# Optimization experiments

Measured on AMD Instinct MI355X. Metric: run time of the kernel, lower is better.

## Reference

```python
import jax, jax.numpy as jnp
import numpy as np

D_MODEL = 2048; D_STATE = 128; D_CONV = 4; EXPAND = 2
HEADDIM = 64; NGROUPS = 1; CHUNK = 256
D_INNER = EXPAND * D_MODEL          # 4096
NHEADS = D_INNER // HEADDIM         # 64
HG = NHEADS // NGROUPS              # heads per group
CONV_DIM = D_INNER + 2 * NGROUPS * D_STATE          # 4352
D_IN_PROJ = 2 * D_INNER + 2 * NGROUPS * D_STATE + NHEADS  # 8512
BATCH = 2; SEQLEN = 2048
EPS = 1e-5


def setup_inputs() -> dict:
    ks = jax.random.split(jax.random.key(0), 8)
    u = jax.random.normal(ks[0], (BATCH, SEQLEN, D_MODEL), jnp.float32)
    in_proj_w = jax.random.normal(ks[1], (D_IN_PROJ, D_MODEL), jnp.float32) * D_MODEL ** -0.5
    conv_w = jax.random.normal(ks[2], (CONV_DIM, D_CONV), jnp.float32) * D_CONV ** -0.5
    conv_b = jax.random.normal(ks[3], (CONV_DIM,), jnp.float32) * 0.1
    # dt_bias init exactly as in the module: inv softplus of dt ~ U(log(1e-3), log(1e-1))
    dt = jnp.exp(jax.random.uniform(ks[4], (NHEADS,), jnp.float32)
                 * (np.float32(np.log(0.1)) - np.float32(np.log(0.001))) + np.float32(np.log(0.001)))
    dt = jnp.clip(dt, 1e-4, None)
    dt_bias = dt + jnp.log(-jnp.expm1(-dt))
    A_log = jnp.log(jax.random.uniform(ks[5], (NHEADS,), jnp.float32, minval=1.0, maxval=16.0))
    D_skip = jnp.ones((NHEADS,), jnp.float32)
    norm_w = jnp.ones((D_INNER,), jnp.float32)
    out_proj_w = jax.random.normal(ks[6], (D_MODEL, D_INNER), jnp.float32) * D_INNER ** -0.5
    return dict(u=u, in_proj_w=in_proj_w, conv_w=conv_w, conv_b=conv_b,
                dt_bias=dt_bias, A_log=A_log, D_skip=D_skip,
                norm_w=norm_w, out_proj_w=out_proj_w)


def _mamba2(u, in_proj_w, conv_w, conv_b, dt_bias, A_log, D_skip, norm_w, out_proj_w):
    b, l, _ = u.shape
    nc = l // CHUNK
    zxbcdt = u @ in_proj_w.T                                   # (b,l,d_in_proj)
    z = zxbcdt[..., :D_INNER]                                  # gate
    xBC = zxbcdt[..., D_INNER:D_INNER + CONV_DIM]
    dt = jax.nn.softplus(zxbcdt[..., D_INNER + CONV_DIM:] + dt_bias)  # (b,l,h)
    # causal depthwise conv1d (padding d_conv-1, truncated to seqlen) + SiLU
    xp = jnp.pad(xBC, ((0, 0), (D_CONV - 1, 0), (0, 0)))
    conv = conv_b + sum(conv_w[:, k] * xp[:, k:k + l, :] for k in range(D_CONV))
    xBC = jax.nn.silu(conv)
    x = xBC[..., :D_INNER].reshape(b, l, NHEADS, HEADDIM)
    Bm = xBC[..., D_INNER:D_INNER + NGROUPS * D_STATE].reshape(b, l, NGROUPS, D_STATE)
    Cm = xBC[..., D_INNER + NGROUPS * D_STATE:].reshape(b, l, NGROUPS, D_STATE)
    A = -jnp.exp(A_log)                                        # (h,)
    # ---- SSD chunked scan ----
    xc = x.reshape(b, nc, CHUNK, NGROUPS, HG, HEADDIM)         # (b,c,s,g,H,p)
    dtc = dt.reshape(b, nc, CHUNK, NGROUPS, HG)                # (b,c,s,g,H)
    Bc = Bm.reshape(b, nc, CHUNK, NGROUPS, D_STATE)            # (b,c,s,g,n)
    Cc = Cm.reshape(b, nc, CHUNK, NGROUPS, D_STATE)
    dA = jnp.transpose(dtc * A.reshape(NGROUPS, HG), (0, 3, 4, 1, 2))  # (b,g,H,c,s)
    dA_cs = jnp.cumsum(dA, axis=-1)                            # (b,g,H,c,s)
    # intra-chunk: L[i,j] = exp(sum_{j<k<=i} dA_k), lower-triangular (diag=1)
    seg = dA_cs[..., :, None] - dA_cs[..., None, :]            # (b,g,H,c,l,s)
    tri = jnp.tril(jnp.ones((CHUNK, CHUNK), bool))
    Lmat = jnp.where(tri, jnp.exp(seg), 0.0)
    xdt = xc * dtc[..., None]                                  # (b,c,s,g,H,p)
    CB = jnp.einsum('bclgn,bcsgn->bcgls', Cc, Bc)
    Y_diag = jnp.einsum('bcgls,bgHcls,bcsgHp->bclgHp', CB, Lmat, xdt)
    # chunk states and inter-chunk recurrence
    decay_states = jnp.exp(dA_cs[..., -1:] - dA_cs)            # (b,g,H,c,s)
    states = jnp.einsum('bcsgn,bgHcs,bcsgHp->bcgHpn', Bc, decay_states, xdt)
    chunk_decay = jnp.exp(dA_cs[..., -1])                      # (b,g,H,c)

    def step(carry, inp):
        st, dec = inp
        return carry * dec[..., None, None] + st, carry

    _, prev = jax.lax.scan(step, jnp.zeros_like(states[:, 0]),
                           (jnp.moveaxis(states, 1, 0), jnp.moveaxis(chunk_decay, -1, 0)))
    prev = jnp.moveaxis(prev, 0, 1)                            # (b,c,g,H,p,n) state entering chunk
    Y_off = jnp.einsum('bclgn,bcgHpn,bgHcl->bclgHp', Cc, prev, jnp.exp(dA_cs))
    y = (Y_diag + Y_off).reshape(b, l, NHEADS, HEADDIM) + x * D_skip[None, None, :, None]
    y = y.reshape(b, l, D_INNER)
    # gated RMSNorm: gate first (norm_before_gate=False), groupwise rms (ngroups=1 -> full)
    y = y * jax.nn.silu(z)
    yg = y.reshape(b, l, NGROUPS, D_INNER // NGROUPS)
    yg = yg * jax.lax.rsqrt(jnp.mean(yg * yg, axis=-1, keepdims=True) + EPS)
    y = yg.reshape(b, l, D_INNER) * norm_w
    return y @ out_proj_w.T                                    # (b,l,d_model)


def reference(u, in_proj_w, conv_w, conv_b, dt_bias, A_log, D_skip, norm_w, out_proj_w):
    return _mamba2(u, in_proj_w, conv_w, conv_b, dt_bias, A_log, D_skip, norm_w, out_proj_w)
```

## Files before the change

kernel.cpp:

```cpp
#include <hip/hip_runtime.h>
#include <hip/hip_bf16.h>


#define D_MODEL   2048
#define D_STATE   128
#define HEADDIM   64
#define CHUNK     256
#define D_INNER   4096
#define NHEADS    64
#define CONV_DIM  4352
#define D_IN_PROJ 8512
#define SEQLEN    2048
#define NC        8
#define ROWSTOT   4096
#define NPAD      8576
#define RMS_EPS   1e-5f

#define OFF_WIN   0ull
#define OFF_XBF   0ull
#define OFF_PREV  0ull
#define OFF_WOUT  16777216ull
#define OFF_UBF   35127296ull
#define OFF_DTV   35127296ull
#define OFF_DACS  36175872ull
#define OFF_BBF   37224448ull
#define OFF_CBF   38273024ull
#define OFF_CB    39321600ull
#define OFF_BT    43515904ull
#define OFF_XBC   51904512ull
#define OFF_STATE 51904512ull
#define OFF_ZBF   87556096ull
#define OFF_DTRAW 121110528ull
#define OFF_YBUF  121110528ull
#define WS_NEEDED 154664960ull

#define N4_U    2097152l
#define N4_WIN  4390912l

typedef __hip_bfloat16 bf16;
typedef __bf16 bfrag8 __attribute__((ext_vector_type(8)));
typedef float  f32x4v __attribute__((ext_vector_type(4)));

__device__ __forceinline__ f32x4v mfma16(bfrag8 a, bfrag8 b, f32x4v c) {
  return __builtin_amdgcn_mfma_f32_16x16x32_bf16(a, b, c, 0, 0, 0);
}

__device__ __forceinline__ void gload_lds16(const void* g, void* l) {
  __builtin_amdgcn_global_load_lds((const __attribute__((address_space(1))) void*)g,
                                   (__attribute__((address_space(3))) void*)l, 16, 0, 0);
}

__device__ __forceinline__ bf16 f2b(float x) { return __float2bfloat16(x); }
__device__ __forceinline__ float b2f(bf16 x) { return __bfloat162float(x); }
__device__ __forceinline__ float siluf(float x) { return x / (1.f + __expf(-x)); }

__global__ __launch_bounds__(256) void cast_all_kernel(const float* __restrict__ u,
    const float* __restrict__ w_in,
    bf16* __restrict__ u_bf, bf16* __restrict__ win_bf) {
  long i = (long)blockIdx.x * 256 + threadIdx.x;
  if (i < N4_U) {
    float4 v = ((const float4*)u)[i];
    bf16* o = u_bf + i * 4;
    o[0] = f2b(v.x); o[1] = f2b(v.y); o[2] = f2b(v.z); o[3] = f2b(v.w);
  } else if (i < N4_U + N4_WIN) {
    long e = (i - N4_U) * 4;
    long row = e / D_MODEL;
    bf16* o = win_bf + e;
    if (row < D_IN_PROJ) {
      float4 v = *(const float4*)(w_in + e);
      o[0] = f2b(v.x); o[1] = f2b(v.y); o[2] = f2b(v.z); o[3] = f2b(v.w);
    } else {
      bf16 z = f2b(0.f);
      o[0] = z; o[1] = z; o[2] = z; o[3] = z;
    }
  }
}

__global__ __launch_bounds__(256) void cast_kernel(const float* __restrict__ in,
                                                   bf16* __restrict__ out, long n4) {
  long i = (long)blockIdx.x * 256 + threadIdx.x;
  if (i >= n4) return;
  float4 v = ((const float4*)in)[i];
  bf16* o = out + i * 4;
  o[0] = f2b(v.x); o[1] = f2b(v.y); o[2] = f2b(v.z); o[3] = f2b(v.w);
}

__global__ __launch_bounds__(512) void gemm1_kernel(const bf16* __restrict__ A,
                                                    const bf16* __restrict__ B,
                                                    bf16* __restrict__ zb,
                                                    bf16* __restrict__ xbc,
                                                    float* __restrict__ dtraw) {
  int pid = blockIdx.x;
  int t = pid & 63, s = pid >> 6;
  int sm = s / 9, sn = s % 9;
  int xcd = t & 7, j8 = t >> 3;
  int tm = sm * 8 + (xcd >> 1) * 2 + (j8 & 1);
  int tn = sn * 8 + (xcd & 1) * 4 + (j8 >> 1);
  if (tn >= 67) return;
  long row0 = (long)tm * 256, col0 = (long)tn * 128;

  __shared__ __align__(16) bf16 As[2 * 256 * 32];
  __shared__ __align__(16) bf16 Bs[2 * 128 * 32];
  int tid = threadIdx.x, lane = tid & 63, w = tid >> 6;
  int wr = w >> 1, wc = w & 1, r16 = lane & 15, q = lane >> 4;
  const int K = D_MODEL;
  f32x4v zero4 = {0.f, 0.f, 0.f, 0.f};
  f32x4v acc[4][4];
#pragma unroll
  for (int i = 0; i < 4; ++i)
#pragma unroll
    for (int j = 0; j < 4; ++j) acc[i][j] = zero4;

  for (int kt = 0; kt < K; kt += 64) {
    __syncthreads();
#pragma unroll
    for (int j = 0; j < 4; ++j) {
      int ci = j * 512 + tid;
      int half = ci >> 10, cj = ci & 1023;
      int r = cj >> 2, ko = half * 32 + (cj & 3) * 8;
      gload_lds16(A + (row0 + r) * (long)K + kt + ko,
                  (char*)As + j * 8192 + w * 1024);
    }
#pragma unroll
    for (int j = 0; j < 2; ++j) {
      int ci = j * 512 + tid;
      int half = ci >> 9, cj = ci & 511;
      int r = cj >> 2, ko = half * 32 + (cj & 3) * 8;
      gload_lds16(B + (col0 + r) * (long)K + kt + ko,
                  (char*)Bs + j * 8192 + w * 1024);
    }
    __syncthreads();
#pragma unroll
    for (int ks = 0; ks < 2; ++ks) {
      const bf16* Ab = As + ks * 8192;
      const bf16* Bb = Bs + ks * 4096;
      bfrag8 af[4], bfv[4];
#pragma unroll
      for (int i = 0; i < 4; ++i) af[i]  = *(const bfrag8*)(Ab + (wr * 64 + i * 16 + r16) * 32 + q * 8);
#pragma unroll
      for (int i = 0; i < 4; ++i) bfv[i] = *(const bfrag8*)(Bb + (wc * 64 + i * 16 + r16) * 32 + q * 8);
#pragma unroll
      for (int i = 0; i < 4; ++i)
#pragma unroll
        for (int j = 0; j < 4; ++j) acc[i][j] = mfma16(af[i], bfv[j], acc[i][j]);
    }
  }
#pragma unroll
  for (int i = 0; i < 4; ++i)
#pragma unroll
    for (int j = 0; j < 4; ++j) {
      long col = col0 + wc * 64 + j * 16 + r16;
#pragma unroll
      for (int r = 0; r < 4; ++r) {
        long row = row0 + wr * 64 + i * 16 + q * 4 + r;
        float v = acc[i][j][r];
        if (col < D_INNER)                       zb[row * D_INNER + col] = f2b(v);
        else if (col < D_INNER + CONV_DIM)       xbc[row * CONV_DIM + (col - D_INNER)] = f2b(v);
        else if (col < D_IN_PROJ)                dtraw[row * NHEADS + (col - D_INNER - CONV_DIM)] = v;
      }
    }
}

__global__ __launch_bounds__(256) void gemm2_kernel(const bf16* __restrict__ A,
                                                    const bf16* __restrict__ B,
                                                    float* __restrict__ C) {
  int pid = blockIdx.x;
  int t = pid & 63, s = pid >> 6;
  int sm = s >> 1, sn = s & 1;
  int xcd = t & 7, j8 = t >> 3;
  int tm = sm * 8 + (xcd >> 1) * 2 + (j8 & 1);
  int tn = sn * 8 + (xcd & 1) * 4 + (j8 >> 1);
  long row0 = (long)tm * 128, col0 = (long)tn * 128;

  __shared__ __align__(16) bf16 As[2 * 128 * 32];
  __shared__ __align__(16) bf16 Bs[2 * 128 * 32];
  int tid = threadIdx.x, lane = tid & 63, w = tid >> 6;
  int wr = w >> 1, wc = w & 1, r16 = lane & 15, q = lane >> 4;
  const int K = D_INNER, ldc = D_MODEL;
  f32x4v zero4 = {0.f, 0.f, 0.f, 0.f};
  f32x4v acc[4][4];
#pragma unroll
  for (int i = 0; i < 4; ++i)
#pragma unroll
    for (int j = 0; j < 4; ++j) acc[i][j] = zero4;

  for (int kt = 0; kt < K; kt += 64) {
    __syncthreads();
#pragma unroll
    for (int j = 0; j < 4; ++j) {
      int ci = (j * 4 + w) * 64 + lane;
      int half = ci >> 9, cj = ci & 511;
      int r = cj >> 2, ko = half * 32 + (cj & 3) * 8;
      gload_lds16(A + (row0 + r) * (long)K + kt + ko,
                  (char*)As + (j * 4 + w) * 1024);
    }
#pragma unroll
    for (int j = 0; j < 4; ++j) {
      int ci = (j * 4 + w) * 64 + lane;
      int half = ci >> 9, cj = ci & 511;
      int r = cj >> 2, ko = half * 32 + (cj & 3) * 8;
      gload_lds16(B + (col0 + r) * (long)K + kt + ko,
                  (char*)Bs + (j * 4 + w) * 1024);
    }
    __syncthreads();
#pragma unroll
    for (int ks = 0; ks < 2; ++ks) {
      const bf16* Ab = As + ks * 4096;
      const bf16* Bb = Bs + ks * 4096;
      bfrag8 af[4], bfv[4];
#pragma unroll
      for (int i = 0; i < 4; ++i) af[i]  = *(const bfrag8*)(Ab + (wr * 64 + i * 16 + r16) * 32 + q * 8);
#pragma unroll
      for (int i = 0; i < 4; ++i) bfv[i] = *(const bfrag8*)(Bb + (wc * 64 + i * 16 + r16) * 32 + q * 8);
#pragma unroll
      for (int i = 0; i < 4; ++i)
#pragma unroll
        for (int j = 0; j < 4; ++j) acc[i][j] = mfma16(af[i], bfv[j], acc[i][j]);
    }
  }
#pragma unroll
  for (int i = 0; i < 4; ++i)
#pragma unroll
    for (int j = 0; j < 4; ++j)
#pragma unroll
      for (int r = 0; r < 4; ++r) {
        long row = row0 + wr * 64 + i * 16 + q * 4 + r;
        long col = col0 + wc * 64 + j * 16 + r16;
        C[row * ldc + col] = acc[i][j][r];
      }
}

__global__ __launch_bounds__(256) void dt_scan_kernel(const float* __restrict__ dtraw,
    const float* __restrict__ dt_bias, const float* __restrict__ A_log,
    float* __restrict__ dtv_buf, float* __restrict__ dacs_buf) {
  int blk = blockIdx.x;
  int c = blk & 7, h = (blk >> 3) & 63, b = blk >> 9;
  int s = threadIdx.x, lane = s & 63, w = s >> 6;
  long row = (long)b * SEQLEN + c * CHUNK + s;
  float raw = dtraw[row * NHEADS + h] + dt_bias[h];
  float dtv = fmaxf(raw, 0.f) + log1pf(__expf(-fabsf(raw)));
  float A = -__expf(A_log[h]);
  float x = dtv * A;
#pragma unroll
  for (int off = 1; off < 64; off <<= 1) {
    float y = __shfl_up(x, off);
    if (lane >= off) x += y;
  }
  __shared__ __align__(16) float wsum[4];
  if (lane == 63) wsum[w] = x;
  __syncthreads();
  float pre = 0.f;
#pragma unroll
  for (int i = 0; i < 4; ++i) pre += (i < w) ? wsum[i] : 0.f;
  long o = ((long)(b * NHEADS + h) * NC + c) * CHUNK + s;
  dtv_buf[o] = dtv;
  dacs_buf[o] = x + pre;
}

__global__ __launch_bounds__(256) void conv_kernel(const bf16* __restrict__ xbc,
    const float* __restrict__ conv_w, const float* __restrict__ conv_b,
    bf16* __restrict__ xo, bf16* __restrict__ Bo, bf16* __restrict__ Co,
    bf16* __restrict__ BT) {
  int cidx = blockIdx.x * 256 + threadIdx.x;
  int l0 = blockIdx.y * 8, b = blockIdx.z;
  float4 wv = *(const float4*)(conv_w + cidx * 4);
  float bias = conv_b[cidx];
  const bf16* base = xbc + (long)b * SEQLEN * CONV_DIM + cidx;
  float win[11];
#pragma unroll
  for (int k = 0; k < 11; ++k) {
    int ls = l0 - 3 + k;
    win[k] = (ls >= 0) ? b2f(base[(long)ls * CONV_DIM]) : 0.f;
  }
  int cgrp = (cidx < D_INNER) ? 0 : ((cidx < D_INNER + D_STATE) ? 1 : 2);
  int n = cidx - D_INNER;
  int n2 = cidx - D_INNER - D_STATE;
  int cch = l0 >> 8;
#pragma unroll
  for (int j = 0; j < 8; ++j) {
    float acc = bias + wv.x * win[j] + wv.y * win[j + 1] + wv.z * win[j + 2] + wv.w * win[j + 3];
    bf16 o = f2b(siluf(acc));
    int l = l0 + j;
    long rowo = (long)b * SEQLEN + l;
    if (cgrp == 0) {
      xo[rowo * D_INNER + cidx] = o;
    } else if (cgrp == 1) {
      Bo[rowo * D_STATE + n] = o;
      BT[(((long)b * NC + cch) * D_STATE + n) * CHUNK + (l & 255)] = o;
    } else {
      Co[rowo * D_STATE + n2] = o;
    }
  }
}

__global__ __launch_bounds__(256) void cb_kernel(const bf16* __restrict__ Cg,
                                                 const bf16* __restrict__ Bg,
                                                 float* __restrict__ CB) {
  int blk = blockIdx.x;
  int stile = blk & 3, bc = blk >> 2;
  int c = bc & 7, b = bc >> 3;
  int tid = threadIdx.x, lane = tid & 63, w = tid >> 6, r16 = lane & 15, q = lane >> 4;
  const bf16* Cb = Cg + ((long)b * SEQLEN + c * CHUNK) * D_STATE;
  const bf16* Bb = Bg + ((long)b * SEQLEN + c * CHUNK) * D_STATE;
  bfrag8 af[4][4];
#pragma unroll
  for (int lt = 0; lt < 4; ++lt)
#pragma unroll
    for (int kk = 0; kk < 4; ++kk)
      af[lt][kk] = *(const bfrag8*)(Cb + (long)(w * 64 + lt * 16 + r16) * D_STATE + kk * 32 + q * 8);
  float* CBb = CB + (long)bc * CHUNK * CHUNK;
  f32x4v zero4 = {0.f, 0.f, 0.f, 0.f};
  for (int st = stile * 4; st < stile * 4 + 4; ++st) {
    f32x4v acc[4] = {zero4, zero4, zero4, zero4};
#pragma unroll
    for (int kk = 0; kk < 4; ++kk) {
      bfrag8 bfv = *(const bfrag8*)(Bb + (long)(st * 16 + r16) * D_STATE + kk * 32 + q * 8);
#pragma unroll
      for (int lt = 0; lt < 4; ++lt) acc[lt] = mfma16(af[lt][kk], bfv, acc[lt]);
    }
#pragma unroll
    for (int lt = 0; lt < 4; ++lt)
#pragma unroll
      for (int r = 0; r < 4; ++r)
        CBb[(long)(w * 64 + lt * 16 + q * 4 + r) * CHUNK + st * 16 + r16] = acc[lt][r];
  }
}

__global__ __launch_bounds__(256) void ssm_diag_kernel(
    const bf16* __restrict__ xg, const bf16* __restrict__ BT,
    const float* __restrict__ CB, const float* __restrict__ dtv_buf,
    const float* __restrict__ dacs_buf, const float* __restrict__ Dskip,
    bf16* __restrict__ ybuf, float* __restrict__ states) {
  int blk = blockIdx.x;
  int h = blk & 63, cc = (blk >> 6) & 7, b = blk >> 9;
  int tid = threadIdx.x, lane = tid & 63, w = tid >> 6, r16 = lane & 15, q = lane >> 4;

  __shared__ __align__(16) __bf16 xT[HEADDIM][264];
  __shared__ __align__(16) float cs_s[CHUNK];
  __shared__ __align__(16) float dt_s[CHUNK];
  __shared__ __align__(16) float w_s[CHUNK];

  long hco = ((long)(b * NHEADS + h) * NC + cc) * CHUNK;
  cs_s[tid] = dacs_buf[hco + tid];
  dt_s[tid] = dtv_buf[hco + tid];
  __syncthreads();
  float cl_last = cs_s[CHUNK - 1];
  w_s[tid] = __expf(cl_last - cs_s[tid]) * dt_s[tid];

  const __bf16* xbase = (const __bf16*)(xg + ((long)b * SEQLEN + cc * CHUNK) * D_INNER + h * HEADDIM);
#pragma unroll
  for (int it = 0; it < 8; ++it) {
    int e = it * 256 + tid;
    int s = e >> 3, p0 = (e & 7) * 8;
    bfrag8 xv = *(const bfrag8*)(xbase + (long)s * D_INNER + p0);
#pragma unroll
    for (int j = 0; j < 8; ++j) xT[p0 + j][s] = xv[j];
  }
  __syncthreads();

  const float* CBchunk = CB + (long)(b * NC + cc) * CHUNK * CHUNK;
  const __bf16* BTc = (const __bf16*)(BT + (((long)b * NC + cc) * D_STATE) * CHUNK);
  f32x4v zero4 = {0.f, 0.f, 0.f, 0.f};
  f32x4v accY[4][4], accS[2][4];
#pragma unroll
  for (int i = 0; i < 4; ++i)
#pragma unroll
    for (int j = 0; j < 4; ++j) accY[i][j] = zero4;
#pragma unroll
  for (int i = 0; i < 2; ++i)
#pragma unroll
    for (int j = 0; j < 4; ++j) accS[i][j] = zero4;

  int l_row[4];
  const float* CBrow[4];
#pragma unroll
  for (int lt = 0; lt < 4; ++lt) {
    l_row[lt] = w * 64 + lt * 16 + r16;
    CBrow[lt] = CBchunk + (long)l_row[lt] * CHUNK;
  }

#pragma unroll 2
  for (int ks = 0; ks < 8; ++ks) {
    int s0 = ks * 32 + q * 8;
    float4 cs0 = *(const float4*)(cs_s + s0);
    float4 cs1 = *(const float4*)(cs_s + s0 + 4);
    float4 dt0 = *(const float4*)(dt_s + s0);
    float4 dt1 = *(const float4*)(dt_s + s0 + 4);
    float4 w0  = *(const float4*)(w_s + s0);
    float4 w1  = *(const float4*)(w_s + s0 + 4);
    float csv[8] = {cs0.x, cs0.y, cs0.z, cs0.w, cs1.x, cs1.y, cs1.z, cs1.w};
    float dtv8[8] = {dt0.x, dt0.y, dt0.z, dt0.w, dt1.x, dt1.y, dt1.z, dt1.w};
    float wv8[8]  = {w0.x, w0.y, w0.z, w0.w, w1.x, w1.y, w1.z, w1.w};

    bfrag8 xf[4];
#pragma unroll
    for (int pt = 0; pt < 4; ++pt) xf[pt] = *(const bfrag8*)(&xT[pt * 16 + r16][s0]);

#pragma unroll
    for (int lt = 0; lt < 4; ++lt) {
      int l = l_row[lt];
      float cs_l = cs_s[l];
      float4 cb0 = *(const float4*)(CBrow[lt] + s0);
      float4 cb1 = *(const float4*)(CBrow[lt] + s0 + 4);
      float cbv[8] = {cb0.x, cb0.y, cb0.z, cb0.w, cb1.x, cb1.y, cb1.z, cb1.w};
      bfrag8 pf;
#pragma unroll
      for (int j = 0; j < 8; ++j) {
        float v = (s0 + j <= l)
                    ? cbv[j] * __expf(fminf(cs_l - csv[j], 0.f)) * dtv8[j]
                    : 0.f;
        pf[j] = (__bf16)v;
      }
#pragma unroll
      for (int pt = 0; pt < 4; ++pt) accY[lt][pt] = mfma16(pf, xf[pt], accY[lt][pt]);
    }

#pragma unroll
    for (int nt = 0; nt < 2; ++nt) {
      int n = w * 32 + nt * 16 + r16;
      bfrag8 braw = *(const bfrag8*)(BTc + (long)n * CHUNK + s0);
      bfrag8 bwf;
#pragma unroll
      for (int j = 0; j < 8; ++j) bwf[j] = (__bf16)((float)braw[j] * wv8[j]);
#pragma unroll
      for (int pt = 0; pt < 4; ++pt) accS[nt][pt] = mfma16(bwf, xf[pt], accS[nt][pt]);
    }
  }

  float dsk = Dskip[h];
  bf16* ybase = ybuf + ((long)b * SEQLEN + cc * CHUNK) * D_INNER + h * HEADDIM;
#pragma unroll
  for (int lt = 0; lt < 4; ++lt)
#pragma unroll
    for (int pt = 0; pt < 4; ++pt)
#pragma unroll
      for (int r = 0; r < 4; ++r) {
        int lrow = w * 64 + lt * 16 + q * 4 + r;
        int pcol = pt * 16 + r16;
        ybase[(long)lrow * D_INNER + pcol] = f2b(accY[lt][pt][r] + (float)xT[pcol][lrow] * dsk);
      }
  float* sbase = states + (long)blk * (HEADDIM * D_STATE);
#pragma unroll
  for (int nt = 0; nt < 2; ++nt)
#pragma unroll
    for (int pt = 0; pt < 4; ++pt)
#pragma unroll
      for (int r = 0; r < 4; ++r)
        sbase[(long)(pt * 16 + r16) * D_STATE + w * 32 + nt * 16 + q * 4 + r] = accS[nt][pt][r];
}

__global__ __launch_bounds__(256) void state_scan_kernel(const float* __restrict__ states,
    const float* __restrict__ dacs, bf16* __restrict__ prevb) {
  int gid = blockIdx.x;
  int et = gid & 31, bh = gid >> 5;
  int h = bh & 63, b = bh >> 6;
  int e = et * 256 + threadIdx.x;
  float dec[NC];
#pragma unroll
  for (int c = 0; c < NC; ++c)
    dec[c] = __expf(dacs[((long)(b * NHEADS + h) * NC + c) * CHUNK + (CHUNK - 1)]);
  float carry = 0.f;
#pragma unroll
  for (int c = 0; c < NC; ++c) {
    long off = ((long)((b * NC + c) * NHEADS + h)) * (HEADDIM * D_STATE) + e;
    prevb[off] = f2b(carry);
    carry = carry * dec[c] + states[off];
  }
}

__global__ __launch_bounds__(256) void yoff_kernel(const bf16* __restrict__ Cg,
    const bf16* __restrict__ prevb, const float* __restrict__ dacs,
    bf16* __restrict__ ybuf) {
  int blk = blockIdx.x;
  int h = blk & 63, cc = (blk >> 6) & 7, b = blk >> 9;
  int tid = threadIdx.x, lane = tid & 63, w = tid >> 6, r16 = lane & 15, q = lane >> 4;
  __shared__ __align__(16) float cs_s[CHUNK];
  cs_s[tid] = dacs[((long)(b * NHEADS + h) * NC + cc) * CHUNK + tid];
  __syncthreads();
  const bf16* Cb = Cg + ((long)b * SEQLEN + cc * CHUNK) * D_STATE;
  const bf16* Pb = prevb + (long)blk * (HEADDIM * D_STATE);
  f32x4v zero4 = {0.f, 0.f, 0.f, 0.f};
  f32x4v acc[4][4];
#pragma unroll
  for (int i = 0; i < 4; ++i)
#pragma unroll
    for (int j = 0; j < 4; ++j) acc[i][j] = zero4;
#pragma unroll
  for (int kk = 0; kk < 4; ++kk) {
    bfrag8 bv[4];
#pragma unroll
    for (int pt = 0; pt < 4; ++pt)
      bv[pt] = *(const bfrag8*)(Pb + (long)(pt * 16 + r16) * D_STATE + kk * 32 + q * 8);
#pragma unroll
    for (int lt = 0; lt < 4; ++lt) {
      bfrag8 av = *(const bfrag8*)(Cb + (long)(w * 64 + lt * 16 + r16) * D_STATE + kk * 32 + q * 8);
#pragma unroll
      for (int pt = 0; pt < 4; ++pt) acc[lt][pt] = mfma16(av, bv[pt], acc[lt][pt]);
    }
  }
  bf16* ybase = ybuf + ((long)b * SEQLEN + cc * CHUNK) * D_INNER + h * HEADDIM;
#pragma unroll
  for (int lt = 0; lt < 4; ++lt)
#pragma unroll
    for (int pt = 0; pt < 4; ++pt)
#pragma unroll
      for (int r = 0; r < 4; ++r) {
        int lrow = w * 64 + lt * 16 + q * 4 + r;
        float ef = __expf(cs_s[lrow]);
        bf16* p = ybase + (long)lrow * D_INNER + pt * 16 + r16;
        *p = f2b(b2f(*p) + acc[lt][pt][r] * ef);
      }
}

__global__ __launch_bounds__(256) void gate_norm_kernel(bf16* __restrict__ ybuf,
    const bf16* __restrict__ zb, const float* __restrict__ norm_w) {
  int row = blockIdx.x, tid = threadIdx.x;
  bf16* y = ybuf + (long)row * D_INNER;
  const bf16* z = zb + (long)row * D_INNER;
  float v[16];
  float ss = 0.f;
#pragma unroll
  for (int i = 0; i < 2; ++i) {
    int e = tid * 16 + i * 8;
    bfrag8 yv = *(const bfrag8*)(y + e);
    bfrag8 zv = *(const bfrag8*)(z + e);
#pragma unroll
    for (int j = 0; j < 8; ++j) {
      float a = (float)yv[j] * siluf((float)zv[j]);
      v[i * 8 + j] = a;
      ss += a * a;
    }
  }
#pragma unroll
  for (int off = 32; off > 0; off >>= 1) ss += __shfl_down(ss, off);
  __shared__ __align__(16) float red[4];
  int lane = tid & 63, w = tid >> 6;
  if (lane == 0) red[w] = ss;
  __syncthreads();
  float tot = red[0] + red[1] + red[2] + red[3];
  float scale = rsqrtf(tot * (1.f / D_INNER) + RMS_EPS);
#pragma unroll
  for (int i = 0; i < 2; ++i) {
    int e = tid * 16 + i * 8;
    float4 w0 = *(const float4*)(norm_w + e);
    float4 w1 = *(const float4*)(norm_w + e + 4);
    bfrag8 o;
    o[0] = (__bf16)(v[i * 8 + 0] * scale * w0.x);
    o[1] = (__bf16)(v[i * 8 + 1] * scale * w0.y);
    o[2] = (__bf16)(v[i * 8 + 2] * scale * w0.z);
    o[3] = (__bf16)(v[i * 8 + 3] * scale * w0.w);
    o[4] = (__bf16)(v[i * 8 + 4] * scale * w1.x);
    o[5] = (__bf16)(v[i * 8 + 5] * scale * w1.y);
    o[6] = (__bf16)(v[i * 8 + 6] * scale * w1.z);
    o[7] = (__bf16)(v[i * 8 + 7] * scale * w1.w);
    *(bfrag8*)(y + e) = o;
  }
}

extern "C" void kernel_launch(void* const* d_in, const int* in_sizes, int n_in,
                              void* d_out, int out_size, void* d_ws, size_t ws_size,
                              hipStream_t stream) {
  if (ws_size < WS_NEEDED) return;

  const float* u       = (const float*)d_in[0];
  const float* w_in    = (const float*)d_in[1];
  const float* conv_w  = (const float*)d_in[2];
  const float* conv_b  = (const float*)d_in[3];
  const float* dt_bias = (const float*)d_in[4];
  const float* A_log   = (const float*)d_in[5];
  const float* Dskip   = (const float*)d_in[6];
  const float* norm_w  = (const float*)d_in[7];
  const float* w_out   = (const float*)d_in[8];
  float* out = (float*)d_out;

  char* ws = (char*)d_ws;
  bf16*  win_bf  = (bf16*)(ws + OFF_WIN);
  bf16*  x_bf    = (bf16*)(ws + OFF_XBF);
  bf16*  prevb   = (bf16*)(ws + OFF_PREV);
  bf16*  wout_bf = (bf16*)(ws + OFF_WOUT);
  bf16*  u_bf    = (bf16*)(ws + OFF_UBF);
  float* dtv     = (float*)(ws + OFF_DTV);
  float* dacs    = (float*)(ws + OFF_DACS);
  bf16*  B_bf    = (bf16*)(ws + OFF_BBF);
  bf16*  C_bf    = (bf16*)(ws + OFF_CBF);
  float* CBb     = (float*)(ws + OFF_CB);
  bf16*  BT_bf   = (bf16*)(ws + OFF_BT);
  bf16*  xbc_bf  = (bf16*)(ws + OFF_XBC);
  float* states  = (float*)(ws + OFF_STATE);
  bf16*  z_bf    = (bf16*)(ws + OFF_ZBF);
  float* dt_raw  = (float*)(ws + OFF_DTRAW);
  bf16*  ybuf    = (bf16*)(ws + OFF_YBUF);

  cast_all_kernel<<<25344, 256, 0, stream>>>(u, w_in, u_bf, win_bf);
  gemm1_kernel<<<1152, 512, 0, stream>>>(u_bf, win_bf, z_bf, xbc_bf, dt_raw);
  dt_scan_kernel<<<1024, 256, 0, stream>>>(dt_raw, dt_bias, A_log, dtv, dacs);
  conv_kernel<<<dim3(17, SEQLEN / 8, 2), 256, 0, stream>>>(xbc_bf, conv_w, conv_b, x_bf, B_bf, C_bf, BT_bf);
  cb_kernel<<<64, 256, 0, stream>>>(C_bf, B_bf, CBb);
  ssm_diag_kernel<<<1024, 256, 0, stream>>>(x_bf, BT_bf, CBb, dtv, dacs, Dskip, ybuf, states);
  state_scan_kernel<<<4096, 256, 0, stream>>>(states, dacs, prevb);
  yoff_kernel<<<1024, 256, 0, stream>>>(C_bf, prevb, dacs, ybuf);
  cast_kernel<<<8192, 256, 0, stream>>>(w_out, wout_bf, (long)D_MODEL * D_INNER / 4);
  gate_norm_kernel<<<ROWSTOT, 256, 0, stream>>>(ybuf, z_bf, norm_w);
  gemm2_kernel<<<512, 256, 0, stream>>>(ybuf, wout_bf, out);
}
```

Measured before the change: 590.5 us.

## Swizzle LDS tiles in both GEMMs and enlarge gemm2 tile to 256x128

Applies an XOR swizzle to the K-chunk offset when staging A and B tiles into shared memory, and applies the matching swizzle when reading fragments. This is meant to cut LDS bank conflicts on the 16-byte fragment reads in both GEMMs. gemm2 is also moved from 128x128 tiles with 256 threads to 256x128 tiles with 512 threads and half as many blocks. The larger tile increases reuse of the B tile, at the cost of fewer workgroups for occupancy and load balance.

```diff
diff --git a/kernel.cpp b/kernel.cpp
--- a/kernel.cpp
+++ b/kernel.cpp
@@ -85,6 +85,7 @@
   o[0] = f2b(v.x); o[1] = f2b(v.y); o[2] = f2b(v.z); o[3] = f2b(v.w);
 }
 
+
 __global__ __launch_bounds__(512) void gemm1_kernel(const bf16* __restrict__ A,
                                                     const bf16* __restrict__ B,
                                                     bf16* __restrict__ zb,
@@ -103,6 +104,7 @@
   __shared__ __align__(16) bf16 Bs[2 * 128 * 32];
   int tid = threadIdx.x, lane = tid & 63, w = tid >> 6;
   int wr = w >> 1, wc = w & 1, r16 = lane & 15, q = lane >> 4;
+  int qs = (q ^ ((r16 >> 1) & 3)) * 8;
   const int K = D_MODEL;
   f32x4v zero4 = {0.f, 0.f, 0.f, 0.f};
   f32x4v acc[4][4];
@@ -117,7 +119,8 @@
     for (int j = 0; j < 4; ++j) {
       int ci = j * 512 + tid;
       int half = ci >> 10, cj = ci & 1023;
-      int r = cj >> 2, ko = half * 32 + (cj & 3) * 8;
+      int r = cj >> 2;
+      int ko = half * 32 + ((cj & 3) ^ ((cj >> 3) & 3)) * 8;
       gload_lds16(A + (row0 + r) * (long)K + kt + ko,
                   (char*)As + j * 8192 + w * 1024);
     }
@@ -125,7 +128,8 @@
     for (int j = 0; j < 2; ++j) {
       int ci = j * 512 + tid;
       int half = ci >> 9, cj = ci & 511;
-      int r = cj >> 2, ko = half * 32 + (cj & 3) * 8;
+      int r = cj >> 2;
+      int ko = half * 32 + ((cj & 3) ^ ((cj >> 3) & 3)) * 8;
       gload_lds16(B + (col0 + r) * (long)K + kt + ko,
                   (char*)Bs + j * 8192 + w * 1024);
     }
@@ -136,9 +140,9 @@
       const bf16* Bb = Bs + ks * 4096;
       bfrag8 af[4], bfv[4];
 #pragma unroll
-      for (int i = 0; i < 4; ++i) af[i]  = *(const bfrag8*)(Ab + (wr * 64 + i * 16 + r16) * 32 + q * 8);
-#pragma unroll
-      for (int i = 0; i < 4; ++i) bfv[i] = *(const bfrag8*)(Bb + (wc * 64 + i * 16 + r16) * 32 + q * 8);
+      for (int i = 0; i < 4; ++i) af[i]  = *(const bfrag8*)(Ab + (wr * 64 + i * 16 + r16) * 32 + qs);
+#pragma unroll
+      for (int i = 0; i < 4; ++i) bfv[i] = *(const bfrag8*)(Bb + (wc * 64 + i * 16 + r16) * 32 + qs);
 #pragma unroll
       for (int i = 0; i < 4; ++i)
 #pragma unroll
@@ -161,7 +165,7 @@
     }
 }
 
-__global__ __launch_bounds__(256) void gemm2_kernel(const bf16* __restrict__ A,
+__global__ __launch_bounds__(512) void gemm2_kernel(const bf16* __restrict__ A,
                                                     const bf16* __restrict__ B,
                                                     float* __restrict__ C) {
   int pid = blockIdx.x;
@@ -170,12 +174,13 @@
   int xcd = t & 7, j8 = t >> 3;
   int tm = sm * 8 + (xcd >> 1) * 2 + (j8 & 1);
   int tn = sn * 8 + (xcd & 1) * 4 + (j8 >> 1);
-  long row0 = (long)tm * 128, col0 = (long)tn * 128;
-
-  __shared__ __align__(16) bf16 As[2 * 128 * 32];
+  long row0 = (long)tm * 256, col0 = (long)tn * 128;
+
+  __shared__ __align__(16) bf16 As[2 * 256 * 32];
   __shared__ __align__(16) bf16 Bs[2 * 128 * 32];
   int tid = threadIdx.x, lane = tid & 63, w = tid >> 6;
   int wr = w >> 1, wc = w & 1, r16 = lane & 15, q = lane >> 4;
+  int qs = (q ^ ((r16 >> 1) & 3)) * 8;
   const int K = D_INNER, ldc = D_MODEL;
   f32x4v zero4 = {0.f, 0.f, 0.f, 0.f};
   f32x4v acc[4][4];
@@ -188,30 +193,32 @@
     __syncthreads();
 #pragma unroll
     for (int j = 0; j < 4; ++j) {
-      int ci = (j * 4 + w) * 64 + lane;
+      int ci = j * 512 + tid;
+      int half = ci >> 10, cj = ci & 1023;
+      int r = cj >> 2;
+      int ko = half * 32 + ((cj & 3) ^ ((cj >> 3) & 3)) * 8;
+      gload_lds16(A + (row0 + r) * (long)K + kt + ko,
+                  (char*)As + j * 8192 + w * 1024);
+    }
+#pragma unroll
+    for (int j = 0; j < 2; ++j) {
+      int ci = j * 512 + tid;
       int half = ci >> 9, cj = ci & 511;
-      int r = cj >> 2, ko = half * 32 + (cj & 3) * 8;
-      gload_lds16(A + (row0 + r) * (long)K + kt + ko,
-                  (char*)As + (j * 4 + w) * 1024);
-    }
-#pragma unroll
-    for (int j = 0; j < 4; ++j) {
-      int ci = (j * 4 + w) * 64 + lane;
-      int half = ci >> 9, cj = ci & 511;
-      int r = cj >> 2, ko = half * 32 + (cj & 3) * 8;
+      int r = cj >> 2;
+      int ko = half * 32 + ((cj & 3) ^ ((cj >> 3) & 3)) * 8;
       gload_lds16(B + (col0 + r) * (long)K + kt + ko,
-                  (char*)Bs + (j * 4 + w) * 1024);
+                  (char*)Bs + j * 8192 + w * 1024);
     }
     __syncthreads();
 #pragma unroll
     for (int ks = 0; ks < 2; ++ks) {
-      const bf16* Ab = As + ks * 4096;
+      const bf16* Ab = As + ks * 8192;
       const bf16* Bb = Bs + ks * 4096;
       bfrag8 af[4], bfv[4];
 #pragma unroll
-      for (int i = 0; i < 4; ++i) af[i]  = *(const bfrag8*)(Ab + (wr * 64 + i * 16 + r16) * 32 + q * 8);
-#pragma unroll
-      for (int i = 0; i < 4; ++i) bfv[i] = *(const bfrag8*)(Bb + (wc * 64 + i * 16 + r16) * 32 + q * 8);
+      for (int i = 0; i < 4; ++i) af[i]  = *(const bfrag8*)(Ab + (wr * 64 + i * 16 + r16) * 32 + qs);
+#pragma unroll
+      for (int i = 0; i < 4; ++i) bfv[i] = *(const bfrag8*)(Bb + (wc * 64 + i * 16 + r16) * 32 + qs);
 #pragma unroll
       for (int i = 0; i < 4; ++i)
 #pragma unroll
@@ -601,5 +608,5 @@
   yoff_kernel<<<1024, 256, 0, stream>>>(C_bf, prevb, dacs, ybuf);
   cast_kernel<<<8192, 256, 0, stream>>>(w_out, wout_bf, (long)D_MODEL * D_INNER / 4);
   gate_norm_kernel<<<ROWSTOT, 256, 0, stream>>>(ybuf, z_bf, norm_w);
-  gemm2_kernel<<<512, 256, 0, stream>>>(ybuf, wout_bf, out);
-}
+  gemm2_kernel<<<256, 512, 0, stream>>>(ybuf, wout_bf, out);
+}
```

Measured after the change: 597.6 us. No clear change (+1.2%).
